# Optimization experiments

Measured on AMD Instinct MI355X. Metric: run time of the kernel, lower is better.

## Reference

```python
import jax, jax.numpy as jnp
import numpy as np

N_NODES = 100000


def gcn_layer(x, W, b, src, dst, n):
    # PyG GCNConv: add self-loops, symmetric degree normalization,
    # message = norm * (x @ W)[src], aggregated (sum) at dst, plus bias.
    loops = jnp.arange(n, dtype=src.dtype)
    s = jnp.concatenate([src, loops])  # [E+N]
    d = jnp.concatenate([dst, loops])  # [E+N]
    deg = jnp.zeros((n,), x.dtype).at[d].add(jnp.ones((s.shape[0],), x.dtype))
    dinv = jnp.where(deg > 0, jax.lax.rsqrt(deg), 0.0)
    norm = dinv[s] * dinv[d]  # [E+N]
    h = x @ W  # [N, out]
    msg = h[s] * norm[:, None]  # [E+N, out]
    out = jax.ops.segment_sum(msg, d, num_segments=n)
    return out + b


def setup_inputs() -> dict:
    key = jax.random.key(0)
    k1, k2, k3, k4 = jax.random.split(key, 4)
    in_dim, hid_dim, out_dim = 128, 128, 64
    x = jax.random.normal(k1, (N_NODES, in_dim), dtype=jnp.float32)
    edge_index = jax.random.randint(k2, (2, 1600000), 0, N_NODES, dtype=jnp.int64)
    W1 = jax.random.normal(k3, (in_dim, hid_dim), dtype=jnp.float32) / np.sqrt(in_dim)
    b1 = jnp.zeros((hid_dim,), jnp.float32)
    W2 = jax.random.normal(k4, (hid_dim, out_dim), dtype=jnp.float32) / np.sqrt(hid_dim)
    b2 = jnp.zeros((out_dim,), jnp.float32)
    return {"x": x, "edge_index": edge_index, "W1": W1, "b1": b1, "W2": W2, "b2": b2}


def reference(x, edge_index, W1, b1, W2, b2):
    src, dst = edge_index[0], edge_index[1]
    h = gcn_layer(x, W1, b1, src, dst, N_NODES)
    h = jax.nn.relu(h)
    # F.dropout(training=False) -> identity (eval mode reference)
    out = gcn_layer(h, W2, b2, src, dst, N_NODES)
    return out
```

## Files before the change

### kernel.cpp

```cpp
#include <hip/hip_runtime.h>
#include <hip/hip_fp16.h>

#define NN 100000
#define NSB 256
#define WPS2 391
#define CAP2 8192
#define EPB 16

typedef _Float16 f16;
typedef _Float16 f16x8 __attribute__((ext_vector_type(8)));
typedef float f32x4 __attribute__((ext_vector_type(4)));

__device__ __forceinline__ int eload(const void* e, long i, int is64) {
  if (is64) return (int)((const long long*)e)[i];
  return ((const int*)e)[i];
}

__global__ __launch_bounds__(1024) void k_detect(const unsigned* __restrict__ e,
                                                 int* __restrict__ flag) {
  __shared__ unsigned red[1024];
  int t = threadIdx.x;
  unsigned acc = e[1 + 2 * t] | e[1 + 2 * t + 2048];
  red[t] = acc;
  __syncthreads();
  for (int off = 512; off > 0; off >>= 1) {
    if (t < off) red[t] |= red[t + off];
    __syncthreads();
  }
  if (t == 0) *flag = (red[0] == 0) ? 1 : 0;
}

__global__ void k_init256(int* __restrict__ bcur2) {
  int i = threadIdx.x;
  bcur2[i] = i * CAP2;
}

__global__ __launch_bounds__(256) void k_split(const void* __restrict__ e,
                                               const int* __restrict__ flag,
                                               int E, int* __restrict__ bcur2,
                                               int* __restrict__ srcb,
                                               int* __restrict__ dstb) {
  __shared__ int hist[NSB];
  const int tid = threadIdx.x;
  const long b0 = (long)blockIdx.x * (256 * EPB);
  const int is64 = *flag;
  hist[tid] = 0;
  __syncthreads();

  int sv[EPB], dv[EPB];
#pragma unroll
  for (int j = 0; j < EPB; ++j) {
    long idx = b0 + j * 256 + tid;
    int s = 0, d = -1;
    if (idx < E) {
      s = eload(e, idx, is64);
      d = eload(e, (long)E + idx, is64);
    }
    sv[j] = s; dv[j] = d;
    if (d >= 0) atomicAdd(&hist[(unsigned)d / WPS2], 1);
  }
  __syncthreads();
  {
    int c = hist[tid];
    int base = (c > 0) ? atomicAdd(&bcur2[tid], c) : 0;
    __syncthreads();
    hist[tid] = base;
  }
  __syncthreads();
#pragma unroll
  for (int j = 0; j < EPB; ++j) {
    int d = dv[j];
    if (d < 0) continue;
    int pos = atomicAdd(&hist[(unsigned)d / WPS2], 1);
    srcb[pos] = sv[j];
    dstb[pos] = d;
  }
}

__global__ __launch_bounds__(256) void k_hist2(const int* __restrict__ dstb,
                                               const int* __restrict__ bcur2,
                                               int* __restrict__ counts,
                                               float* __restrict__ dinv) {
  __shared__ int lc[WPS2];
  const int b = blockIdx.x;
  const int nlo = b * WPS2;
  const int nhi = (nlo + WPS2 < NN) ? nlo + WPS2 : NN;
  const int nw = nhi - nlo;
  for (int j = threadIdx.x; j < nw; j += 256) lc[j] = 0;
  __syncthreads();
  const int cnt = bcur2[b] - b * CAP2;
  const long s0 = (long)b * CAP2;
  for (int i = threadIdx.x; i < cnt; i += 256)
    atomicAdd(&lc[dstb[s0 + i] - nlo], 1);
  __syncthreads();
  for (int j = threadIdx.x; j < nw; j += 256) {
    int c = lc[j];
    counts[nlo + j] = c;
    dinv[nlo + j] = rsqrtf((float)c + 1.0f);
  }
}

__global__ __launch_bounds__(256) void k_scatter2(const int* __restrict__ dstb,
                                                  const int* __restrict__ srcb,
                                                  const int* __restrict__ bcur2,
                                                  const int* __restrict__ rowptr,
                                                  int* __restrict__ csr) {
  __shared__ int cur[WPS2];
  const int b = blockIdx.x;
  const int nlo = b * WPS2;
  const int nhi = (nlo + WPS2 < NN) ? nlo + WPS2 : NN;
  const int nw = nhi - nlo;
  for (int j = threadIdx.x; j < nw; j += 256) cur[j] = rowptr[nlo + j];
  __syncthreads();
  const int cnt = bcur2[b] - b * CAP2;
  const long s0 = (long)b * CAP2;
  for (int i = threadIdx.x; i < cnt; i += 256) {
    int d = dstb[s0 + i];
    int pos = atomicAdd(&cur[d - nlo], 1);
    csr[pos] = srcb[s0 + i];
  }
}

__global__ __launch_bounds__(512) void k_scan1(const int* __restrict__ counts,
                                               int* __restrict__ rowptr,
                                               int* __restrict__ bsum) {
  __shared__ int sm[512];
  int tid = threadIdx.x;
  int i = blockIdx.x * 512 + tid;
  int v = (i < NN) ? counts[i] : 0;
  sm[tid] = v;
  __syncthreads();
  for (int off = 1; off < 512; off <<= 1) {
    int t = (tid >= off) ? sm[tid - off] : 0;
    __syncthreads();
    sm[tid] += t;
    __syncthreads();
  }
  if (i < NN) rowptr[i] = sm[tid] - v;
  if (tid == 511) bsum[blockIdx.x] = sm[tid];
}

__global__ void k_scan2(int* __restrict__ bsum, int nb) {
  if (threadIdx.x == 0 && blockIdx.x == 0) {
    int run = 0;
    for (int b = 0; b < nb; ++b) { int v = bsum[b]; bsum[b] = run; run += v; }
  }
}

__global__ __launch_bounds__(512) void k_scan3(int* __restrict__ rowptr,
                                               const int* __restrict__ bsum, int E) {
  int i = blockIdx.x * 512 + threadIdx.x;
  if (i < NN) rowptr[i] += bsum[blockIdx.x];
  if (i == 0) rowptr[NN] = E;
}

template <int COUT>
__global__ void k_wprep(const float* __restrict__ W, f16* __restrict__ Wt) {
  int idx = blockIdx.x * 256 + threadIdx.x;
  if (idx < 128 * COUT) {
    int k = idx / COUT, n = idx % COUT;
    Wt[n * 128 + k] = (f16)W[idx];
  }
}

template <int COUT, bool RELU, typename TIN>
__global__ __launch_bounds__(256) void gemm_mfma(const TIN* __restrict__ X,
                                                 const f16* __restrict__ Wt,
                                                 const float* __restrict__ dinv,
                                                 f16* __restrict__ Y) {
  constexpr int NF = COUT / 16;
  __shared__ f16 Al[128 * 128];
  __shared__ f16 Bl[COUT * 128];
  const int tid = threadIdx.x;
  const long row0 = (long)blockIdx.x * 128;

  for (int c = tid; c < COUT * 16; c += 256) {
    int n = c >> 4, g = c & 15;
    f16x8 v = *(const f16x8*)&Wt[n * 128 + g * 8];
    *(f16x8*)((char*)Bl + n * 256 + ((g * 16) ^ ((n & 7) << 4))) = v;
  }
  for (int c = tid; c < 2048; c += 256) {
    int r = c >> 4, g = c & 15;
    long grow = row0 + r;
    f16x8 v;
    if (grow < NN) {
      if constexpr (sizeof(TIN) == 4) {
        const float4* p = (const float4*)&X[grow * 128 + g * 8];
        float4 p0 = p[0], p1 = p[1];
        float f[8] = {p0.x, p0.y, p0.z, p0.w, p1.x, p1.y, p1.z, p1.w};
#pragma unroll
        for (int j = 0; j < 8; ++j) {
          float t = RELU ? fmaxf(f[j], 0.f) : f[j];
          v[j] = (f16)t;
        }
      } else {
        v = *(const f16x8*)&X[grow * 128 + g * 8];
        if (RELU) {
#pragma unroll
          for (int j = 0; j < 8; ++j) v[j] = v[j] > (f16)0 ? v[j] : (f16)0;
        }
      }
    } else {
#pragma unroll
      for (int j = 0; j < 8; ++j) v[j] = (f16)0;
    }
    *(f16x8*)((char*)Al + r * 256 + ((g * 16) ^ ((r & 7) << 4))) = v;
  }
  __syncthreads();

  const int l = tid & 63, w = tid >> 6;
  const int lm = l & 15, lg = l >> 4;
  const int r0 = w * 32 + lm, r1 = r0 + 16;

  f32x4 acc0[NF], acc1[NF];
#pragma unroll
  for (int nf = 0; nf < NF; ++nf) {
    acc0[nf] = (f32x4)(0.f);
    acc1[nf] = (f32x4)(0.f);
  }

#pragma unroll
  for (int kk = 0; kk < 4; ++kk) {
    const int kb = kk * 64 + lg * 16;
    f16x8 a0 = *(const f16x8*)((const char*)Al + r0 * 256 + (kb ^ ((r0 & 7) << 4)));
    f16x8 a1 = *(const f16x8*)((const char*)Al + r1 * 256 + (kb ^ ((r1 & 7) << 4)));
#pragma unroll
    for (int nf = 0; nf < NF; ++nf) {
      int n = nf * 16 + lm;
      f16x8 b = *(const f16x8*)((const char*)Bl + n * 256 + (kb ^ ((n & 7) << 4)));
      acc0[nf] = __builtin_amdgcn_mfma_f32_16x16x32_f16(a0, b, acc0[nf], 0, 0, 0);
      acc1[nf] = __builtin_amdgcn_mfma_f32_16x16x32_f16(a1, b, acc1[nf], 0, 0, 0);
    }
  }

#pragma unroll
  for (int reg = 0; reg < 4; ++reg) {
    long gr0 = row0 + w * 32 + lg * 4 + reg;
    long gr1 = gr0 + 16;
    float d0 = (gr0 < NN) ? dinv[gr0] : 0.f;
    float d1 = (gr1 < NN) ? dinv[gr1] : 0.f;
#pragma unroll
    for (int nf = 0; nf < NF; ++nf) {
      if (gr0 < NN) Y[gr0 * COUT + nf * 16 + lm] = (f16)(acc0[nf][reg] * d0);
      if (gr1 < NN) Y[gr1 * COUT + nf * 16 + lm] = (f16)(acc1[nf][reg] * d1);
    }
  }
}

template <int C, typename TOUT>
__global__ __launch_bounds__(256) void k_agg_csr(const __half* __restrict__ hn,
                                                 const int* __restrict__ rowptr,
                                                 const int* __restrict__ csr,
                                                 const float* __restrict__ dinv,
                                                 const float* __restrict__ bias,
                                                 TOUT* __restrict__ out) {
  constexpr int TP = C / 8;
  long t = (long)blockIdx.x * 256 + threadIdx.x;
  int d = (int)(t / TP);
  if (d >= NN) return;
  int c8 = (int)(t % TP) * 8;

  float acc[8];
  {
    float4 raw = *(const float4*)&hn[(long)d * C + c8];
    const __half2* h2 = (const __half2*)&raw;
#pragma unroll
    for (int q = 0; q < 4; ++q) {
      float2 f = __half22float2(h2[q]);
      acc[2 * q] = f.x; acc[2 * q + 1] = f.y;
    }
  }
  int e = rowptr[d];
  const int end = rowptr[d + 1];

  for (; e + 4 <= end; e += 4) {
    int s0 = csr[e], s1 = csr[e + 1], s2 = csr[e + 2], s3 = csr[e + 3];
    float4 r0 = *(const float4*)&hn[(long)s0 * C + c8];
    float4 r1 = *(const float4*)&hn[(long)s1 * C + c8];
    float4 r2 = *(const float4*)&hn[(long)s2 * C + c8];
    float4 r3 = *(const float4*)&hn[(long)s3 * C + c8];
    const __half2* a0 = (const __half2*)&r0;
    const __half2* a1 = (const __half2*)&r1;
    const __half2* a2 = (const __half2*)&r2;
    const __half2* a3 = (const __half2*)&r3;
#pragma unroll
    for (int q = 0; q < 4; ++q) {
      float2 f0 = __half22float2(a0[q]);
      float2 f1 = __half22float2(a1[q]);
      float2 f2 = __half22float2(a2[q]);
      float2 f3 = __half22float2(a3[q]);
      acc[2 * q]     += (f0.x + f1.x) + (f2.x + f3.x);
      acc[2 * q + 1] += (f0.y + f1.y) + (f2.y + f3.y);
    }
  }
  for (; e < end; ++e) {
    int s = csr[e];
    float4 r0 = *(const float4*)&hn[(long)s * C + c8];
    const __half2* a0 = (const __half2*)&r0;
#pragma unroll
    for (int q = 0; q < 4; ++q) {
      float2 f0 = __half22float2(a0[q]);
      acc[2 * q] += f0.x; acc[2 * q + 1] += f0.y;
    }
  }

  float dd = dinv[d];
  float4 b0 = *(const float4*)&bias[c8];
  float4 b1 = *(const float4*)&bias[c8 + 4];
  float o[8];
  o[0] = acc[0] * dd + b0.x; o[1] = acc[1] * dd + b0.y;
  o[2] = acc[2] * dd + b0.z; o[3] = acc[3] * dd + b0.w;
  o[4] = acc[4] * dd + b1.x; o[5] = acc[5] * dd + b1.y;
  o[6] = acc[6] * dd + b1.z; o[7] = acc[7] * dd + b1.w;

  if constexpr (sizeof(TOUT) == 2) {
    __half2 hp[4];
    hp[0] = __floats2half2_rn(o[0], o[1]);
    hp[1] = __floats2half2_rn(o[2], o[3]);
    hp[2] = __floats2half2_rn(o[4], o[5]);
    hp[3] = __floats2half2_rn(o[6], o[7]);
    *(float4*)&out[(long)d * C + c8] = *(float4*)hp;
  } else {
    *(float4*)&out[(long)d * C + c8]     = make_float4(o[0], o[1], o[2], o[3]);
    *(float4*)&out[(long)d * C + c8 + 4] = make_float4(o[4], o[5], o[6], o[7]);
  }
}

extern "C" void kernel_launch(void* const* d_in, const int* in_sizes, int n_in,
                              void* d_out, int out_size, void* d_ws, size_t ws_size,
                              hipStream_t stream) {
  const float* x  = (const float*)d_in[0];
  const void*  ep = d_in[1];
  const float* W1 = (const float*)d_in[2];
  const float* b1 = (const float*)d_in[3];
  const float* W2 = (const float*)d_in[4];
  const float* b2 = (const float*)d_in[5];
  float* out = (float*)d_out;
  const int E = in_sizes[1] / 2;

  float*  wsf    = (float*)d_ws;
  int*    wsi    = (int*)d_ws;
  int*    flag   = wsi;
  int*    bcur2  = wsi + 16;
  float*  dinv   = wsf + 512;
  int*    counts = wsi + 100512;
  int*    rowptr = wsi + 200512;
  int*    bsum   = wsi + 300544;
  f16*    Wt1    = (f16*)(wsi + 300800);
  f16*    Wt2    = (f16*)(wsi + 308992);
  int*    csr    = wsi + 313088;
  int*    srcb   = wsi + 1913088;
  int*    dstb   = wsi + 4010240;
  f16*    hn1    = (f16*)(wsi + 1913088);
  f16*    a1     = (f16*)(wsi + 8313088);
  f16*    hn2    = hn1;

  const int NB = (NN + 511) / 512;
  const int SB = (E + 256 * EPB - 1) / (256 * EPB);
  const int GB = (NN + 127) / 128;

  k_detect<<<1, 1024, 0, stream>>>((const unsigned*)ep, flag);
  k_init256<<<1, NSB, 0, stream>>>(bcur2);
  k_wprep<128><<<64, 256, 0, stream>>>(W1, Wt1);
  k_wprep<64><<<32, 256, 0, stream>>>(W2, Wt2);
  k_split<<<SB, 256, 0, stream>>>(ep, flag, E, bcur2, srcb, dstb);
  k_hist2<<<NSB, 256, 0, stream>>>(dstb, bcur2, counts, dinv);
  k_scan1<<<NB, 512, 0, stream>>>(counts, rowptr, bsum);
  k_scan2<<<1, 64, 0, stream>>>(bsum, NB);
  k_scan3<<<NB, 512, 0, stream>>>(rowptr, bsum, E);
  k_scatter2<<<NSB, 256, 0, stream>>>(dstb, srcb, bcur2, rowptr, csr);

  gemm_mfma<128, false, float><<<GB, 256, 0, stream>>>(x, Wt1, dinv, hn1);
  k_agg_csr<128, __half><<<(NN * 16) / 256, 256, 0, stream>>>(
      (const __half*)hn1, rowptr, csr, dinv, b1, (__half*)a1);

  gemm_mfma<64, true, f16><<<GB, 256, 0, stream>>>(a1, Wt2, dinv, hn2);
  k_agg_csr<64, float><<<(NN * 8) / 256, 256, 0, stream>>>(
      (const __half*)hn2, rowptr, csr, dinv, b2, out);
}
```

Before: 225.5 us.

## Fuse CSR build stages and fuse layer-1 aggregation with layer-2 GEMM

Merges the init and weight-prep kernels, and replaces the histogram, three-stage global scan and scatter with one per-bucket scan plus a single build kernel that computes local prefix sums, rowptr, dinv and the CSR fill. The first-layer aggregation is fused with bias, ReLU and the second-layer MFMA GEMM, so the intermediate activation never goes to global memory. The final aggregation gains 8-way unrolled gathers. This cuts launches and global traffic. The cost is lower occupancy in the fused kernel, and per-block sequential aggregation may expose gather latency.

New measurement: 193.5 us. 1.17x faster.

```diff
diff --git a/kernel.cpp b/kernel.cpp
--- a/kernel.cpp
+++ b/kernel.cpp
@@ -17,9 +17,11 @@
 }
 
 __global__ __launch_bounds__(1024) void k_detect(const unsigned* __restrict__ e,
-                                                 int* __restrict__ flag) {
+                                                 int* __restrict__ flag,
+                                                 int* __restrict__ bcur2) {
   __shared__ unsigned red[1024];
   int t = threadIdx.x;
+  if (t < NSB) bcur2[t] = t * CAP2;
   unsigned acc = e[1 + 2 * t] | e[1 + 2 * t + 2048];
   red[t] = acc;
   __syncthreads();
@@ -30,9 +32,19 @@
   if (t == 0) *flag = (red[0] == 0) ? 1 : 0;
 }
 
-__global__ void k_init256(int* __restrict__ bcur2) {
-  int i = threadIdx.x;
-  bcur2[i] = i * CAP2;
+__global__ void k_wprep(const float* __restrict__ W1, const float* __restrict__ W2,
+                        f16* __restrict__ Wt1, f16* __restrict__ Wt2) {
+  int idx = blockIdx.x * 256 + threadIdx.x;
+  if (idx < 128 * 128) {
+    int k = idx / 128, n = idx % 128;
+    Wt1[n * 128 + k] = (f16)W1[idx];
+  } else {
+    int i2 = idx - 128 * 128;
+    if (i2 < 128 * 64) {
+      int k = i2 / 64, n = i2 % 64;
+      Wt2[n * 128 + k] = (f16)W2[i2];
+    }
+  }
 }
 
 __global__ __launch_bounds__(256) void k_split(const void* __restrict__ e,
@@ -77,104 +89,84 @@
   }
 }
 
-__global__ __launch_bounds__(256) void k_hist2(const int* __restrict__ dstb,
+__global__ __launch_bounds__(256) void k_wscan(const int* __restrict__ bcur2,
+                                               int* __restrict__ wbase,
+                                               int* __restrict__ rowptr, int E) {
+  __shared__ int sm[NSB];
+  int t = threadIdx.x;
+  int c = bcur2[t] - t * CAP2;
+  sm[t] = c;
+  __syncthreads();
+  for (int off = 1; off < NSB; off <<= 1) {
+    int a = (t >= off) ? sm[t - off] : 0;
+    __syncthreads();
+    sm[t] += a;
+    __syncthreads();
+  }
+  wbase[t] = sm[t] - c;
+  if (t == 0) rowptr[NN] = E;
+}
+
+__global__ __launch_bounds__(256) void k_build(const int* __restrict__ dstb,
+                                               const int* __restrict__ srcb,
                                                const int* __restrict__ bcur2,
-                                               int* __restrict__ counts,
-                                               float* __restrict__ dinv) {
-  __shared__ int lc[WPS2];
+                                               const int* __restrict__ wbase,
+                                               int* __restrict__ rowptr,
+                                               float* __restrict__ dinv,
+                                               int* __restrict__ csr) {
+  __shared__ int lc[512];
+  __shared__ int cur[512];
+  const int tid = threadIdx.x;
   const int b = blockIdx.x;
   const int nlo = b * WPS2;
   const int nhi = (nlo + WPS2 < NN) ? nlo + WPS2 : NN;
   const int nw = nhi - nlo;
-  for (int j = threadIdx.x; j < nw; j += 256) lc[j] = 0;
+  lc[tid] = 0; lc[tid + 256] = 0;
   __syncthreads();
   const int cnt = bcur2[b] - b * CAP2;
   const long s0 = (long)b * CAP2;
-  for (int i = threadIdx.x; i < cnt; i += 256)
+  for (int i = tid; i < cnt; i += 256)
     atomicAdd(&lc[dstb[s0 + i] - nlo], 1);
   __syncthreads();
-  for (int j = threadIdx.x; j < nw; j += 256) {
-    int c = lc[j];
-    counts[nlo + j] = c;
-    dinv[nlo + j] = rsqrtf((float)c + 1.0f);
-  }
-}
-
-__global__ __launch_bounds__(256) void k_scatter2(const int* __restrict__ dstb,
-                                                  const int* __restrict__ srcb,
-                                                  const int* __restrict__ bcur2,
-                                                  const int* __restrict__ rowptr,
-                                                  int* __restrict__ csr) {
-  __shared__ int cur[WPS2];
-  const int b = blockIdx.x;
-  const int nlo = b * WPS2;
-  const int nhi = (nlo + WPS2 < NN) ? nlo + WPS2 : NN;
-  const int nw = nhi - nlo;
-  for (int j = threadIdx.x; j < nw; j += 256) cur[j] = rowptr[nlo + j];
-  __syncthreads();
-  const int cnt = bcur2[b] - b * CAP2;
-  const long s0 = (long)b * CAP2;
-  for (int i = threadIdx.x; i < cnt; i += 256) {
+  for (int off = 1; off < 512; off <<= 1) {
+    int a0 = (tid >= off) ? lc[tid - off] : 0;
+    int a1 = (tid + 256 >= off) ? lc[tid + 256 - off] : 0;
+    __syncthreads();
+    lc[tid] += a0; lc[tid + 256] += a1;
+    __syncthreads();
+  }
+  const int wb = wbase[b];
+#pragma unroll
+  for (int h = 0; h < 2; ++h) {
+    int j = tid + h * 256;
+    if (j < nw) {
+      int inc = lc[j];
+      int c = inc - (j > 0 ? lc[j - 1] : 0);
+      int ex = wb + inc - c;
+      rowptr[nlo + j] = ex;
+      dinv[nlo + j] = rsqrtf((float)c + 1.0f);
+      cur[j] = ex;
+    }
+  }
+  __syncthreads();
+  for (int i = tid; i < cnt; i += 256) {
     int d = dstb[s0 + i];
     int pos = atomicAdd(&cur[d - nlo], 1);
     csr[pos] = srcb[s0 + i];
   }
 }
 
-__global__ __launch_bounds__(512) void k_scan1(const int* __restrict__ counts,
-                                               int* __restrict__ rowptr,
-                                               int* __restrict__ bsum) {
-  __shared__ int sm[512];
-  int tid = threadIdx.x;
-  int i = blockIdx.x * 512 + tid;
-  int v = (i < NN) ? counts[i] : 0;
-  sm[tid] = v;
-  __syncthreads();
-  for (int off = 1; off < 512; off <<= 1) {
-    int t = (tid >= off) ? sm[tid - off] : 0;
-    __syncthreads();
-    sm[tid] += t;
-    __syncthreads();
-  }
-  if (i < NN) rowptr[i] = sm[tid] - v;
-  if (tid == 511) bsum[blockIdx.x] = sm[tid];
-}
-
-__global__ void k_scan2(int* __restrict__ bsum, int nb) {
-  if (threadIdx.x == 0 && blockIdx.x == 0) {
-    int run = 0;
-    for (int b = 0; b < nb; ++b) { int v = bsum[b]; bsum[b] = run; run += v; }
-  }
-}
-
-__global__ __launch_bounds__(512) void k_scan3(int* __restrict__ rowptr,
-                                               const int* __restrict__ bsum, int E) {
-  int i = blockIdx.x * 512 + threadIdx.x;
-  if (i < NN) rowptr[i] += bsum[blockIdx.x];
-  if (i == 0) rowptr[NN] = E;
-}
-
-template <int COUT>
-__global__ void k_wprep(const float* __restrict__ W, f16* __restrict__ Wt) {
-  int idx = blockIdx.x * 256 + threadIdx.x;
-  if (idx < 128 * COUT) {
-    int k = idx / COUT, n = idx % COUT;
-    Wt[n * 128 + k] = (f16)W[idx];
-  }
-}
-
-template <int COUT, bool RELU, typename TIN>
-__global__ __launch_bounds__(256) void gemm_mfma(const TIN* __restrict__ X,
+__global__ __launch_bounds__(256) void gemm_mfma(const float* __restrict__ X,
                                                  const f16* __restrict__ Wt,
                                                  const float* __restrict__ dinv,
                                                  f16* __restrict__ Y) {
-  constexpr int NF = COUT / 16;
+  constexpr int NF = 8;
   __shared__ f16 Al[128 * 128];
-  __shared__ f16 Bl[COUT * 128];
+  __shared__ f16 Bl[128 * 128];
   const int tid = threadIdx.x;
   const long row0 = (long)blockIdx.x * 128;
 
-  for (int c = tid; c < COUT * 16; c += 256) {
+  for (int c = tid; c < 128 * 16; c += 256) {
     int n = c >> 4, g = c & 15;
     f16x8 v = *(const f16x8*)&Wt[n * 128 + g * 8];
     *(f16x8*)((char*)Bl + n * 256 + ((g * 16) ^ ((n & 7) << 4))) = v;
@@ -184,22 +176,11 @@
     long grow = row0 + r;
     f16x8 v;
     if (grow < NN) {
-      if constexpr (sizeof(TIN) == 4) {
-        const float4* p = (const float4*)&X[grow * 128 + g * 8];
-        float4 p0 = p[0], p1 = p[1];
-        float f[8] = {p0.x, p0.y, p0.z, p0.w, p1.x, p1.y, p1.z, p1.w};
-#pragma unroll
-        for (int j = 0; j < 8; ++j) {
-          float t = RELU ? fmaxf(f[j], 0.f) : f[j];
-          v[j] = (f16)t;
-        }
-      } else {
-        v = *(const f16x8*)&X[grow * 128 + g * 8];
-        if (RELU) {
-#pragma unroll
-          for (int j = 0; j < 8; ++j) v[j] = v[j] > (f16)0 ? v[j] : (f16)0;
-        }
-      }
+      const float4* p = (const float4*)&X[grow * 128 + g * 8];
+      float4 p0 = p[0], p1 = p[1];
+      float f[8] = {p0.x, p0.y, p0.z, p0.w, p1.x, p1.y, p1.z, p1.w};
+#pragma unroll
+      for (int j = 0; j < 8; ++j) v[j] = (f16)f[j];
     } else {
 #pragma unroll
       for (int j = 0; j < 8; ++j) v[j] = (f16)0;
@@ -214,10 +195,7 @@
 
   f32x4 acc0[NF], acc1[NF];
 #pragma unroll
-  for (int nf = 0; nf < NF; ++nf) {
-    acc0[nf] = (f32x4)(0.f);
-    acc1[nf] = (f32x4)(0.f);
-  }
+  for (int nf = 0; nf < NF; ++nf) { acc0[nf] = (f32x4)(0.f); acc1[nf] = (f32x4)(0.f); }
 
 #pragma unroll
   for (int kk = 0; kk < 4; ++kk) {
@@ -241,20 +219,118 @@
     float d1 = (gr1 < NN) ? dinv[gr1] : 0.f;
 #pragma unroll
     for (int nf = 0; nf < NF; ++nf) {
-      if (gr0 < NN) Y[gr0 * COUT + nf * 16 + lm] = (f16)(acc0[nf][reg] * d0);
-      if (gr1 < NN) Y[gr1 * COUT + nf * 16 + lm] = (f16)(acc1[nf][reg] * d1);
-    }
-  }
-}
-
-template <int C, typename TOUT>
-__global__ __launch_bounds__(256) void k_agg_csr(const __half* __restrict__ hn,
-                                                 const int* __restrict__ rowptr,
-                                                 const int* __restrict__ csr,
-                                                 const float* __restrict__ dinv,
-                                                 const float* __restrict__ bias,
-                                                 TOUT* __restrict__ out) {
-  constexpr int TP = C / 8;
+      if (gr0 < NN) Y[gr0 * 128 + nf * 16 + lm] = (f16)(acc0[nf][reg] * d0);
+      if (gr1 < NN) Y[gr1 * 128 + nf * 16 + lm] = (f16)(acc1[nf][reg] * d1);
+    }
+  }
+}
+
+__global__ __launch_bounds__(256) void k_aggemm(const f16* __restrict__ hn1,
+                                                const int* __restrict__ rowptr,
+                                                const int* __restrict__ csr,
+                                                const float* __restrict__ dinv,
+                                                const float* __restrict__ b1,
+                                                const f16* __restrict__ Wt2,
+                                                f16* __restrict__ hn2) {
+  __shared__ f16 Al[64 * 128];
+  __shared__ f16 Bl[64 * 128];
+  const int tid = threadIdx.x;
+  const long row0 = (long)blockIdx.x * 64;
+
+  for (int c = tid; c < 64 * 16; c += 256) {
+    int n = c >> 4, g = c & 15;
+    f16x8 v = *(const f16x8*)&Wt2[n * 128 + g * 8];
+    *(f16x8*)((char*)Bl + n * 256 + ((g * 16) ^ ((n & 7) << 4))) = v;
+  }
+
+  const int g = tid & 15;
+  const int c8 = g * 8;
+  const int rloc = tid >> 4;
+  float4 bb0 = *(const float4*)&b1[c8];
+  float4 bb1 = *(const float4*)&b1[c8 + 4];
+  const float bb[8] = {bb0.x, bb0.y, bb0.z, bb0.w, bb1.x, bb1.y, bb1.z, bb1.w};
+
+#pragma unroll
+  for (int p = 0; p < 4; ++p) {
+    int r = p * 16 + rloc;
+    long dd = row0 + r;
+    f16x8 v;
+    if (dd < NN) {
+      float acc[8];
+      f16x8 sv = *(const f16x8*)&hn1[dd * 128 + c8];
+#pragma unroll
+      for (int j = 0; j < 8; ++j) acc[j] = (float)sv[j];
+      int e = rowptr[dd];
+      const int end = rowptr[dd + 1];
+      for (; e + 4 <= end; e += 4) {
+        int s0 = csr[e], s1 = csr[e + 1], s2 = csr[e + 2], s3 = csr[e + 3];
+        f16x8 v0 = *(const f16x8*)&hn1[(long)s0 * 128 + c8];
+        f16x8 v1 = *(const f16x8*)&hn1[(long)s1 * 128 + c8];
+        f16x8 v2 = *(const f16x8*)&hn1[(long)s2 * 128 + c8];
+        f16x8 v3 = *(const f16x8*)&hn1[(long)s3 * 128 + c8];
+#pragma unroll
+        for (int j = 0; j < 8; ++j)
+          acc[j] += ((float)v0[j] + (float)v1[j]) + ((float)v2[j] + (float)v3[j]);
+      }
+      for (; e < end; ++e) {
+        int s = csr[e];
+        f16x8 v0 = *(const f16x8*)&hn1[(long)s * 128 + c8];
+#pragma unroll
+        for (int j = 0; j < 8; ++j) acc[j] += (float)v0[j];
+      }
+      float ddv = dinv[dd];
+#pragma unroll
+      for (int j = 0; j < 8; ++j) {
+        float t = fmaxf(acc[j] * ddv + bb[j], 0.f);
+        v[j] = (f16)t;
+      }
+    } else {
+#pragma unroll
+      for (int j = 0; j < 8; ++j) v[j] = (f16)0;
+    }
+    *(f16x8*)((char*)Al + r * 256 + ((g * 16) ^ ((r & 7) << 4))) = v;
+  }
+  __syncthreads();
+
+  const int l = tid & 63, w = tid >> 6;
+  const int lm = l & 15, lg = l >> 4;
+  const int r0 = w * 16 + lm;
+
+  f32x4 acc0[4];
+#pragma unroll
+  for (int nf = 0; nf < 4; ++nf) acc0[nf] = (f32x4)(0.f);
+
+#pragma unroll
+  for (int kk = 0; kk < 4; ++kk) {
+    const int kb = kk * 64 + lg * 16;
+    f16x8 a0 = *(const f16x8*)((const char*)Al + r0 * 256 + (kb ^ ((r0 & 7) << 4)));
+#pragma unroll
+    for (int nf = 0; nf < 4; ++nf) {
+      int n = nf * 16 + lm;
+      f16x8 b = *(const f16x8*)((const char*)Bl + n * 256 + (kb ^ ((n & 7) << 4)));
+      acc0[nf] = __builtin_amdgcn_mfma_f32_16x16x32_f16(a0, b, acc0[nf], 0, 0, 0);
+    }
+  }
+
+#pragma unroll
+  for (int reg = 0; reg < 4; ++reg) {
+    long gr0 = row0 + w * 16 + lg * 4 + reg;
+    if (gr0 < NN) {
+      float d0 = dinv[gr0];
+#pragma unroll
+      for (int nf = 0; nf < 4; ++nf)
+        hn2[gr0 * 64 + nf * 16 + lm] = (f16)(acc0[nf][reg] * d0);
+    }
+  }
+}
+
+__global__ __launch_bounds__(256) void k_agg2(const __half* __restrict__ hn,
+                                              const int* __restrict__ rowptr,
+                                              const int* __restrict__ csr,
+                                              const float* __restrict__ dinv,
+                                              const float* __restrict__ bias,
+                                              float* __restrict__ out) {
+  constexpr int C = 64, TP = 8;
   long t = (long)blockIdx.x * 256 + threadIdx.x;
   int d = (int)(t / TP);
   if (d >= NN) return;
@@ -273,29 +349,36 @@
   int e = rowptr[d];
   const int end = rowptr[d + 1];
 
+  for (; e + 8 <= end; e += 8) {
+    float4 r[8];
+#pragma unroll
+    for (int u = 0; u < 8; ++u) r[u] = *(const float4*)&hn[(long)csr[e + u] * C + c8];
+#pragma unroll
+    for (int u = 0; u < 8; ++u) {
+      const __half2* a0 = (const __half2*)&r[u];
+#pragma unroll
+      for (int q = 0; q < 4; ++q) {
+        float2 f0 = __half22float2(a0[q]);
+        acc[2 * q] += f0.x; acc[2 * q + 1] += f0.y;
+      }
+    }
+  }
   for (; e + 4 <= end; e += 4) {
-    int s0 = csr[e], s1 = csr[e + 1], s2 = csr[e + 2], s3 = csr[e + 3];
-    float4 r0 = *(const float4*)&hn[(long)s0 * C + c8];
-    float4 r1 = *(const float4*)&hn[(long)s1 * C + c8];
-    float4 r2 = *(const float4*)&hn[(long)s2 * C + c8];
-    float4 r3 = *(const float4*)&hn[(long)s3 * C + c8];
-    const __half2* a0 = (const __half2*)&r0;
-    const __half2* a1 = (const __half2*)&r1;
-    const __half2* a2 = (const __half2*)&r2;
-    const __half2* a3 = (const __half2*)&r3;
-#pragma unroll
-    for (int q = 0; q < 4; ++q) {
-      float2 f0 = __half22float2(a0[q]);
-      float2 f1 = __half22float2(a1[q]);
-      float2 f2 = __half22float2(a2[q]);
-      float2 f3 = __half22float2(a3[q]);
-      acc[2 * q]     += (f0.x + f1.x) + (f2.x + f3.x);
-      acc[2 * q + 1] += (f0.y + f1.y) + (f2.y + f3.y);
+    float4 r[4];
+#pragma unroll
+    for (int u = 0; u < 4; ++u) r[u] = *(const float4*)&hn[(long)csr[e + u] * C + c8];
+#pragma unroll
+    for (int u = 0; u < 4; ++u) {
+      const __half2* a0 = (const __half2*)&r[u];
+#pragma unroll
+      for (int q = 0; q < 4; ++q) {
+        float2 f0 = __half22float2(a0[q]);
+        acc[2 * q] += f0.x; acc[2 * q + 1] += f0.y;
+      }
     }
   }
   for (; e < end; ++e) {
-    int s = csr[e];
-    float4 r0 = *(const float4*)&hn[(long)s * C + c8];
+    float4 r0 = *(const float4*)&hn[(long)csr[e] * C + c8];
     const __half2* a0 = (const __half2*)&r0;
 #pragma unroll
     for (int q = 0; q < 4; ++q) {
@@ -307,23 +390,12 @@
   float dd = dinv[d];
   float4 b0 = *(const float4*)&bias[c8];
   float4 b1 = *(const float4*)&bias[c8 + 4];
-  float o[8];
-  o[0] = acc[0] * dd + b0.x; o[1] = acc[1] * dd + b0.y;
-  o[2] = acc[2] * dd + b0.z; o[3] = acc[3] * dd + b0.w;
-  o[4] = acc[4] * dd + b1.x; o[5] = acc[5] * dd + b1.y;
-  o[6] = acc[6] * dd + b1.z; o[7] = acc[7] * dd + b1.w;
-
-  if constexpr (sizeof(TOUT) == 2) {
-    __half2 hp[4];
-    hp[0] = __floats2half2_rn(o[0], o[1]);
-    hp[1] = __floats2half2_rn(o[2], o[3]);
-    hp[2] = __floats2half2_rn(o[4], o[5]);
-    hp[3] = __floats2half2_rn(o[6], o[7]);
-    *(float4*)&out[(long)d * C + c8] = *(float4*)hp;
-  } else {
-    *(float4*)&out[(long)d * C + c8]     = make_float4(o[0], o[1], o[2], o[3]);
-    *(float4*)&out[(long)d * C + c8 + 4] = make_float4(o[4], o[5], o[6], o[7]);
-  }
+  *(float4*)&out[(long)d * C + c8] =
+      make_float4(acc[0] * dd + b0.x, acc[1] * dd + b0.y,
+                  acc[2] * dd + b0.z, acc[3] * dd + b0.w);
+  *(float4*)&out[(long)d * C + c8 + 4] =
+      make_float4(acc[4] * dd + b1.x, acc[5] * dd + b1.y,
+                  acc[6] * dd + b1.z, acc[7] * dd + b1.w);
 }
 
 extern "C" void kernel_launch(void* const* d_in, const int* in_sizes, int n_in,
@@ -341,40 +413,30 @@
   float*  wsf    = (float*)d_ws;
   int*    wsi    = (int*)d_ws;
   int*    flag   = wsi;
-  int*    bcur2  = wsi + 16;
-  float*  dinv   = wsf + 512;
-  int*    counts = wsi + 100512;
-  int*    rowptr = wsi + 200512;
-  int*    bsum   = wsi + 300544;
-  f16*    Wt1    = (f16*)(wsi + 300800);
-  f16*    Wt2    = (f16*)(wsi + 308992);
-  int*    csr    = wsi + 313088;
-  int*    srcb   = wsi + 1913088;
-  int*    dstb   = wsi + 4010240;
-  f16*    hn1    = (f16*)(wsi + 1913088);
-  f16*    a1     = (f16*)(wsi + 8313088);
-  f16*    hn2    = hn1;
-
-  const int NB = (NN + 511) / 512;
+  int*    bcur2  = wsi + 64;
+  int*    wbase  = wsi + 320;
+  float*  dinv   = wsf + 576;
+  int*    rowptr = wsi + 100576;
+  f16*    Wt1    = (f16*)(wsi + 200640);
+  f16*    Wt2    = (f16*)(wsi + 208832);
+  int*    csr    = wsi + 212992;
+  int*    srcb   = wsi + 1812992;
+  int*    dstb   = wsi + 3910144;
+  f16*    hn1    = (f16*)(wsi + 6007296);
+  f16*    hn2    = (f16*)(wsi + 12407296);
+
   const int SB = (E + 256 * EPB - 1) / (256 * EPB);
   const int GB = (NN + 127) / 128;
-
-  k_detect<<<1, 1024, 0, stream>>>((const unsigned*)ep, flag);
-  k_init256<<<1, NSB, 0, stream>>>(bcur2);
-  k_wprep<128><<<64, 256, 0, stream>>>(W1, Wt1);
-  k_wprep<64><<<32, 256, 0, stream>>>(W2, Wt2);
+  const int FB = (NN + 63) / 64;
+
+  k_detect<<<1, 1024, 0, stream>>>((const unsigned*)ep, flag, bcur2);
+  k_wprep<<<96, 256, 0, stream>>>(W1, W2, Wt1, Wt2);
   k_split<<<SB, 256, 0, stream>>>(ep, flag, E, bcur2, srcb, dstb);
-  k_hist2<<<NSB, 256, 0, stream>>>(dstb, bcur2, counts, dinv);
-  k_scan1<<<NB, 512, 0, stream>>>(counts, rowptr, bsum);
-  k_scan2<<<1, 64, 0, stream>>>(bsum, NB);
-  k_scan3<<<NB, 512, 0, stream>>>(rowptr, bsum, E);
-  k_scatter2<<<NSB, 256, 0, stream>>>(dstb, srcb, bcur2, rowptr, csr);
-
-  gemm_mfma<128, false, float><<<GB, 256, 0, stream>>>(x, Wt1, dinv, hn1);
-  k_agg_csr<128, __half><<<(NN * 16) / 256, 256, 0, stream>>>(
-      (const __half*)hn1, rowptr, csr, dinv, b1, (__half*)a1);
-
-  gemm_mfma<64, true, f16><<<GB, 256, 0, stream>>>(a1, Wt2, dinv, hn2);
-  k_agg_csr<64, float><<<(NN * 8) / 256, 256, 0, stream>>>(
+  k_wscan<<<1, 256, 0, stream>>>(bcur2, wbase, rowptr, E);
+  k_build<<<NSB, 256, 0, stream>>>(dstb, srcb, bcur2, wbase, rowptr, dinv, csr);
+
+  gemm_mfma<<<GB, 256, 0, stream>>>(x, Wt1, dinv, hn1);
+  k_aggemm<<<FB, 256, 0, stream>>>(hn1, rowptr, csr, dinv, b1, Wt2, hn2);
+  k_agg2<<<(NN * 8 + 255) / 256, 256, 0, stream>>>(
       (const __half*)hn2, rowptr, csr, dinv, b2, out);
 }
```
